# Kernel optimization log

Measured on AMD Instinct MI355X. Metric: run time of the kernel, lower is better.

## Reference

```python
import jax, jax.numpy as jnp
import numpy as np

B, T, D_MODEL, HEAD = 4, 4096, 1024, 64

def setup_inputs() -> dict:
    key = jax.random.key(0)
    ks = jax.random.split(key, 7)
    s = 0.02  # typical init scale
    return {
        "x":  jax.random.normal(ks[0], (B, T, D_MODEL), dtype=jnp.float32),
        "Wq": jax.random.normal(ks[1], (D_MODEL, HEAD), dtype=jnp.float32) * s,
        "bq": jnp.zeros((HEAD,), dtype=jnp.float32),
        "Wk": jax.random.normal(ks[2], (D_MODEL, HEAD), dtype=jnp.float32) * s,
        "bk": jnp.zeros((HEAD,), dtype=jnp.float32),
        "Wv": jax.random.normal(ks[3], (D_MODEL, HEAD), dtype=jnp.float32) * s,
        "bv": jnp.zeros((HEAD,), dtype=jnp.float32),
    }

def reference(x, Wq, bq, Wk, bk, Wv, bv):
    Bz, Tz, C = x.shape
    q = x @ Wq + bq                      # (B,T,H)
    k = x @ Wk + bk                      # (B,T,H)
    v = x @ Wv + bv                      # (B,T,H)
    # NOTE: original scales by sqrt(C) = sqrt(d_model), not sqrt(head_size)
    att = jnp.einsum("bth,bsh->bts", q, k) / jnp.sqrt(jnp.float32(C))
    causal = jnp.tril(jnp.ones((Tz, Tz), dtype=bool))
    att = jnp.where(causal, att, -jnp.inf)
    att = jax.nn.softmax(att, axis=-1)
    return jnp.einsum("bts,bsh->bth", att, v)  # (B,T,H)
```

## Files before the change

kernel.cpp:

```cpp
#include <hip/hip_runtime.h>
#include <hip/hip_bf16.h>
#include <hip/hip_fp16.h>

#define T_SEQ 4096
#define DMODEL 1024
#define HEAD 64
#define NBATCH 4
#define NSEG 576
#define S2LOG 0.04508422f

typedef __attribute__((ext_vector_type(8))) short bf16x8;
typedef __attribute__((ext_vector_type(4))) float f32x4;

__device__ __forceinline__ unsigned short f2bf(float f) {
    unsigned int b = __float_as_uint(f);
    unsigned int r = b + 0x7FFFu + ((b >> 16) & 1u);
    return (unsigned short)(r >> 16);
}
__device__ __forceinline__ unsigned int pk_bf16(float a, float b) {
    __hip_bfloat162 h = __float22bfloat162_rn(make_float2(a, b));
    unsigned int u; __builtin_memcpy(&u, &h, 4); return u;
}

__global__ __launch_bounds__(256) void prep_w(
    const float* __restrict__ Wq, const float* __restrict__ Wk,
    const float* __restrict__ Wv, unsigned short* __restrict__ Wtb)
{
    __shared__ unsigned short tl[64 * 72];
    const int bid = blockIdx.x;
    const int m   = bid >> 4;
    const int k0  = (bid & 15) * 64;
    const float* W = (m == 0) ? Wq : (m == 1) ? Wk : Wv;
    const int t  = threadIdx.x;
    const int kr = t >> 2, qtr = t & 3;
#pragma unroll
    for (int i = 0; i < 4; ++i) {
        float4 wv4 = *(const float4*)&W[(k0 + kr) * 64 + qtr * 16 + i * 4];
        tl[(qtr * 16 + i * 4 + 0) * 72 + kr] = f2bf(wv4.x);
        tl[(qtr * 16 + i * 4 + 1) * 72 + kr] = f2bf(wv4.y);
        tl[(qtr * 16 + i * 4 + 2) * 72 + kr] = f2bf(wv4.z);
        tl[(qtr * 16 + i * 4 + 3) * 72 + kr] = f2bf(wv4.w);
    }
    __syncthreads();
#pragma unroll
    for (int c = 0; c < 2; ++c) {
        const int lin = c * 256 + t;
        const int n = lin >> 3, k8 = lin & 7;
        *(uint4*)&Wtb[((long)(m * 64 + n)) * 1024 + k0 + k8 * 8] =
            *(const uint4*)&tl[n * 72 + k8 * 8];
    }
}

__global__ __launch_bounds__(256, 2) void qkv_mfma(
    const float* __restrict__ x, const unsigned short* __restrict__ Wtb,
    const float* __restrict__ bq, const float* __restrict__ bk,
    const float* __restrict__ bv,
    unsigned short* __restrict__ qo, unsigned short* __restrict__ ko,
    unsigned short* __restrict__ vt)
{
    __shared__ __align__(16) unsigned short x_s[2][32 * 136];
    const int t    = threadIdx.x;
    const int lane = t & 63;
    const int l15  = lane & 15, quad = lane >> 4;
    const int w    = __builtin_amdgcn_readfirstlane(t >> 6);
    const long row0 = (long)blockIdx.x * 32;

    float bias[3];
#pragma unroll
    for (int ntl = 0; ntl < 3; ++ntl) {
        const int c = w * 48 + ntl * 16 + l15;
        bias[ntl] = (c < 64) ? bq[c] : (c < 128) ? bk[c - 64] : bv[c - 128];
    }
    f32x4 acc[2][3];
#pragma unroll
    for (int mt = 0; mt < 2; ++mt)
#pragma unroll
        for (int ntl = 0; ntl < 3; ++ntl)
            acc[mt][ntl] = (f32x4){bias[ntl], bias[ntl], bias[ntl], bias[ntl]};

    const int srow = t >> 3, sseg = t & 7;
    const float* xp = x + (row0 + srow) * DMODEL + sseg * 16;

    float4 xv[4];
#pragma unroll
    for (int i = 0; i < 4; ++i) xv[i] = *(const float4*)(xp + i * 4);
    {
        unsigned int pk_[8];
#pragma unroll
        for (int i = 0; i < 4; ++i) {
            pk_[i * 2]     = pk_bf16(xv[i].x, xv[i].y);
            pk_[i * 2 + 1] = pk_bf16(xv[i].z, xv[i].w);
        }
        *(uint4*)&x_s[0][srow * 136 + sseg * 16]     = *(const uint4*)&pk_[0];
        *(uint4*)&x_s[0][srow * 136 + sseg * 16 + 8] = *(const uint4*)&pk_[4];
    }
    __syncthreads();

    for (int sg = 0; sg < 8; ++sg) {
        if (sg + 1 < 8)
#pragma unroll
            for (int i = 0; i < 4; ++i)
                xv[i] = *(const float4*)(xp + (sg + 1) * 128 + i * 4);
        bf16x8 wf[3][4];
#pragma unroll
        for (int ntl = 0; ntl < 3; ++ntl)
#pragma unroll
            for (int kq = 0; kq < 4; ++kq)
                wf[ntl][kq] = *(const bf16x8*)&Wtb[((long)(w * 48 + ntl * 16 + l15)) * 1024
                                                   + sg * 128 + kq * 32 + quad * 8];
#pragma unroll
        for (int mt = 0; mt < 2; ++mt)
#pragma unroll
            for (int kq = 0; kq < 4; ++kq) {
                bf16x8 a = *(const bf16x8*)&x_s[sg & 1][(mt * 16 + l15) * 136 + kq * 32 + quad * 8];
#pragma unroll
                for (int ntl = 0; ntl < 3; ++ntl)
                    acc[mt][ntl] = __builtin_amdgcn_mfma_f32_16x16x32_bf16(a, wf[ntl][kq], acc[mt][ntl], 0, 0, 0);
            }
        if (sg + 1 < 8) {
            unsigned int pk_[8];
#pragma unroll
            for (int i = 0; i < 4; ++i) {
                pk_[i * 2]     = pk_bf16(xv[i].x, xv[i].y);
                pk_[i * 2 + 1] = pk_bf16(xv[i].z, xv[i].w);
            }
            *(uint4*)&x_s[(sg + 1) & 1][srow * 136 + sseg * 16]     = *(const uint4*)&pk_[0];
            *(uint4*)&x_s[(sg + 1) & 1][srow * 136 + sseg * 16 + 8] = *(const uint4*)&pk_[4];
        }
        __syncthreads();
    }
#pragma unroll
    for (int mt = 0; mt < 2; ++mt)
#pragma unroll
        for (int ntl = 0; ntl < 3; ++ntl) {
            const int c = w * 48 + ntl * 16 + l15;
            const long tr0 = row0 + mt * 16 + quad * 4;
            if (c < 64) {
#pragma unroll
                for (int r = 0; r < 4; ++r)
                    qo[(tr0 + r) * HEAD + c] = f2bf(acc[mt][ntl][r] * S2LOG);
            } else if (c < 128) {
#pragma unroll
                for (int r = 0; r < 4; ++r)
                    ko[(tr0 + r) * HEAD + (c - 64)] = f2bf(acc[mt][ntl][r]);
            } else {
                const int b = (int)(tr0 >> 12), tloc = (int)(tr0 & 4095);
                uint2 pv;
                pv.x = pk_bf16(acc[mt][ntl][0], acc[mt][ntl][1]);
                pv.y = pk_bf16(acc[mt][ntl][2], acc[mt][ntl][3]);
                *(uint2*)&vt[((long)(b * HEAD + (c - 128))) * T_SEQ + tloc] = pv;
            }
        }
}

__global__ __launch_bounds__(256, 3) void flash_seg(
    const unsigned short* __restrict__ qg,
    const unsigned short* __restrict__ kg,
    const unsigned short* __restrict__ vtg,
    __half* __restrict__ opart, float* __restrict__ ml)
{
    __shared__ __align__(16) unsigned short p_s[4][32 * 72];
    const int t0   = threadIdx.x;
    const int lane = t0 & 63;
    const int l15  = lane & 15, quad = lane >> 4;
    const int wv   = __builtin_amdgcn_readfirstlane(t0 >> 6);

    const int sid = (NSEG - 1) - (int)blockIdx.x;
    int kk = 0, pref = 0;
#pragma unroll
    for (int i = 0; i < 7; ++i) {
        const int cnt = 16 * (kk + 1);
        if (sid >= pref + cnt) { pref += cnt; ++kk; }
    }
    const int S   = kk + 1;
    const int rem = sid - pref;
    const int t   = kk * 16 + rem / S;
    const int si  = rem % S;
    const int r0  = t * 32;
    const int nck = (t + 2) >> 1;
    const int c0  = (si * nck) / S, c1 = ((si + 1) * nck) / S;
    const int b   = wv;
    const long bbase = (long)b * T_SEQ;
    const int gidx = b * NSEG + sid;

    bf16x8 qf[2][2];
#pragma unroll
    for (int s = 0; s < 2; ++s)
#pragma unroll
        for (int h = 0; h < 2; ++h)
            qf[s][h] = *(const bf16x8*)&qg[(bbase + r0 + s * 16 + l15) * HEAD + h * 32 + quad * 8];

    f32x4 o[2][4];
#pragma unroll
    for (int s = 0; s < 2; ++s)
#pragma unroll
        for (int dt = 0; dt < 4; ++dt) o[s][dt] = (f32x4){0.f, 0.f, 0.f, 0.f};
    float mrun[2] = {-30000.f, -30000.f}, lrun[2] = {0.f, 0.f};

    unsigned short* ps = p_s[wv];

    for (int c = c0; c < c1; ++c) {
        const int key0 = c * 64;
        bf16x8 kf[4][2];
#pragma unroll
        for (int mt = 0; mt < 4; ++mt) {
            int krow = key0 + mt * 16 + l15; if (krow > T_SEQ - 1) krow = T_SEQ - 1;
            const unsigned short* kp = &kg[(bbase + krow) * HEAD + quad * 8];
            kf[mt][0] = *(const bf16x8*)kp;
            kf[mt][1] = *(const bf16x8*)(kp + 32);
        }
        f32x4 st[2][4];
#pragma unroll
        for (int s = 0; s < 2; ++s)
#pragma unroll
            for (int mt = 0; mt < 4; ++mt) {
                f32x4 z = (f32x4){0.f, 0.f, 0.f, 0.f};
                z = __builtin_amdgcn_mfma_f32_16x16x32_bf16(kf[mt][0], qf[s][0], z, 0, 0, 0);
                st[s][mt] = __builtin_amdgcn_mfma_f32_16x16x32_bf16(kf[mt][1], qf[s][1], z, 0, 0, 0);
            }
        bf16x8 vf[4][2];
#pragma unroll
        for (int dt = 0; dt < 4; ++dt)
#pragma unroll
            for (int g = 0; g < 2; ++g) {
                int kof = key0 + g * 32 + quad * 8; if (kof > T_SEQ - 8) kof = T_SEQ - 8;
                vf[dt][g] = *(const bf16x8*)&vtg[((long)(b * HEAD + dt * 16 + l15)) * T_SEQ + kof];
            }
        if (key0 + 63 > r0) {
#pragma unroll
            for (int s = 0; s < 2; ++s) {
                const int row = r0 + s * 16 + l15;
#pragma unroll
                for (int mt = 0; mt < 4; ++mt)
#pragma unroll
                    for (int r = 0; r < 4; ++r) {
                        const int key = key0 + mt * 16 + quad * 4 + r;
                        st[s][mt][r] = (key <= row) ? st[s][mt][r] : -30000.f;
                    }
            }
        }
#pragma unroll
        for (int s = 0; s < 2; ++s) {
            float mx = st[s][0][0];
#pragma unroll
            for (int mt = 0; mt < 4; ++mt)
#pragma unroll
                for (int r = 0; r < 4; ++r) mx = fmaxf(mx, st[s][mt][r]);
            mx = fmaxf(mx, __shfl_xor(mx, 16));
            mx = fmaxf(mx, __shfl_xor(mx, 32));
            const float mn = fmaxf(mrun[s], mx);
            const float al = exp2f(mrun[s] - mn);
            mrun[s] = mn;
            float psum = 0.f;
#pragma unroll
            for (int mt = 0; mt < 4; ++mt) {
                float e0 = exp2f(st[s][mt][0] - mn), e1 = exp2f(st[s][mt][1] - mn);
                float e2 = exp2f(st[s][mt][2] - mn), e3 = exp2f(st[s][mt][3] - mn);
                psum += (e0 + e1) + (e2 + e3);
                *(unsigned int*)&ps[(s * 16 + l15) * 72 + mt * 16 + quad * 4]     = pk_bf16(e0, e1);
                *(unsigned int*)&ps[(s * 16 + l15) * 72 + mt * 16 + quad * 4 + 2] = pk_bf16(e2, e3);
            }
            psum += __shfl_xor(psum, 16);
            psum += __shfl_xor(psum, 32);
            lrun[s] = lrun[s] * al + psum;
#pragma unroll
            for (int dt = 0; dt < 4; ++dt)
#pragma unroll
                for (int r = 0; r < 4; ++r) o[s][dt][r] *= al;
        }
        __builtin_amdgcn_wave_barrier();
        bf16x8 pf[2][2];
#pragma unroll
        for (int s = 0; s < 2; ++s)
#pragma unroll
            for (int g = 0; g < 2; ++g)
                pf[s][g] = *(const bf16x8*)&ps[(s * 16 + l15) * 72 + g * 32 + quad * 8];
        __builtin_amdgcn_wave_barrier();
#pragma unroll
        for (int s = 0; s < 2; ++s)
#pragma unroll
            for (int dt = 0; dt < 4; ++dt) {
                o[s][dt] = __builtin_amdgcn_mfma_f32_16x16x32_bf16(vf[dt][0], pf[s][0], o[s][dt], 0, 0, 0);
                o[s][dt] = __builtin_amdgcn_mfma_f32_16x16x32_bf16(vf[dt][1], pf[s][1], o[s][dt], 0, 0, 0);
            }
    }
    __half* op = opart + (long)gidx * 2048;
#pragma unroll
    for (int s = 0; s < 2; ++s) {
#pragma unroll
        for (int dt = 0; dt < 4; ++dt) {
            __half2 h0 = __floats2half2_rn(o[s][dt][0], o[s][dt][1]);
            __half2 h1 = __floats2half2_rn(o[s][dt][2], o[s][dt][3]);
            uint2 u; __builtin_memcpy(&u.x, &h0, 4); __builtin_memcpy(&u.y, &h1, 4);
            *(uint2*)&op[(s * 16 + l15) * HEAD + dt * 16 + quad * 4] = u;
        }
        if (quad == 0) {
            ml[(long)gidx * 64 + s * 16 + l15]      = mrun[s];
            ml[(long)gidx * 64 + 32 + s * 16 + l15] = lrun[s];
        }
    }
}

__global__ __launch_bounds__(256) void merge_seg(
    const __half* __restrict__ opart, const float* __restrict__ ml,
    float* __restrict__ out)
{
    const int bid = blockIdx.x;
    const int t = bid & 127, b = bid >> 7;
    const int kk = t >> 4, S = kk + 1;
    const int base_sid = 8 * kk * (kk + 1) + (t & 15) * S;
    const int tid = threadIdx.x;
    const int row = tid >> 3, col0 = (tid & 7) * 8;

    float m[8], l[8], M = -30000.f;
    for (int si = 0; si < S; ++si) {
        const long g = (long)(b * NSEG + base_sid + si);
        m[si] = ml[g * 64 + row];
        l[si] = ml[g * 64 + 32 + row];
        M = fmaxf(M, m[si]);
    }
    float acc[8];
#pragma unroll
    for (int j = 0; j < 8; ++j) acc[j] = 0.f;
    float L = 0.f;
    for (int si = 0; si < S; ++si) {
        const float wgt = exp2f(m[si] - M);
        L += wgt * l[si];
        const __half* op = opart + (long)(b * NSEG + base_sid + si) * 2048 + row * 64 + col0;
        uint4 u = *(const uint4*)op;
        __half2 h01, h23, h45, h67;
        __builtin_memcpy(&h01, &u.x, 4); __builtin_memcpy(&h23, &u.y, 4);
        __builtin_memcpy(&h45, &u.z, 4); __builtin_memcpy(&h67, &u.w, 4);
        float2 f01 = __half22float2(h01), f23 = __half22float2(h23);
        float2 f45 = __half22float2(h45), f67 = __half22float2(h67);
        acc[0] += wgt * f01.x; acc[1] += wgt * f01.y;
        acc[2] += wgt * f23.x; acc[3] += wgt * f23.y;
        acc[4] += wgt * f45.x; acc[5] += wgt * f45.y;
        acc[6] += wgt * f67.x; acc[7] += wgt * f67.y;
    }
    const float inv = 1.f / L;
    float4 o0 = {acc[0] * inv, acc[1] * inv, acc[2] * inv, acc[3] * inv};
    float4 o1 = {acc[4] * inv, acc[5] * inv, acc[6] * inv, acc[7] * inv};
    float* dst = out + ((long)(b * T_SEQ + t * 32 + row)) * HEAD + col0;
    *(float4*)dst = o0;
    *(float4*)(dst + 4) = o1;
}

extern "C" void kernel_launch(void* const* d_in, const int* in_sizes, int n_in,
                              void* d_out, int out_size, void* d_ws, size_t ws_size,
                              hipStream_t stream) {
    const float* x  = (const float*)d_in[0];
    const float* Wq = (const float*)d_in[1];
    const float* bq = (const float*)d_in[2];
    const float* Wk = (const float*)d_in[3];
    const float* bk = (const float*)d_in[4];
    const float* Wv = (const float*)d_in[5];
    const float* bv = (const float*)d_in[6];
    float* outp = (float*)d_out;

    char* wsb = (char*)d_ws;
    unsigned short* wtb = (unsigned short*)(wsb);
    unsigned short* qw  = (unsigned short*)(wsb + 393216);
    unsigned short* kw  = (unsigned short*)(wsb + 2490368);
    unsigned short* vtw = (unsigned short*)(wsb + 4587520);
    __half* opart       = (__half*)(wsb + 6684672);
    float*  mlp         = (float*)(wsb + 16121856);

    prep_w<<<dim3(48), dim3(256), 0, stream>>>(Wq, Wk, Wv, wtb);
    qkv_mfma<<<dim3(512), dim3(256), 0, stream>>>(
        x, wtb, bq, bk, bv, qw, kw, vtw);
    flash_seg<<<dim3(NSEG), dim3(256), 0, stream>>>(qw, kw, vtw, opart, mlp);
    merge_seg<<<dim3(512), dim3(256), 0, stream>>>(opart, mlp, outp);
}
```

Measured before the change: 177.3 us.

## Stage x and K/V tiles via direct global-to-LDS DMA and retile flash attention

```diff
diff --git a/kernel.cpp b/kernel.cpp
--- a/kernel.cpp
+++ b/kernel.cpp
@@ -6,7 +6,7 @@
 #define DMODEL 1024
 #define HEAD 64
 #define NBATCH 4
-#define NSEG 576
+#define NSEG 544
 #define S2LOG 0.04508422f
 
 typedef __attribute__((ext_vector_type(8))) short bf16x8;
@@ -20,6 +20,11 @@
 __device__ __forceinline__ unsigned int pk_bf16(float a, float b) {
     __hip_bfloat162 h = __float22bfloat162_rn(make_float2(a, b));
     unsigned int u; __builtin_memcpy(&u, &h, 4); return u;
+}
+__device__ __forceinline__ void dma16(const void* g, void* s) {
+    __builtin_amdgcn_global_load_lds(
+        (const __attribute__((address_space(1))) unsigned int*)g,
+        (__attribute__((address_space(3))) unsigned int*)s, 16, 0, 0);
 }
 
 __global__ __launch_bounds__(256) void prep_w(
@@ -51,14 +56,14 @@
     }
 }
 
-__global__ __launch_bounds__(256, 2) void qkv_mfma(
+__global__ __launch_bounds__(256, 3) void qkv_mfma(
     const float* __restrict__ x, const unsigned short* __restrict__ Wtb,
     const float* __restrict__ bq, const float* __restrict__ bk,
     const float* __restrict__ bv,
     unsigned short* __restrict__ qo, unsigned short* __restrict__ ko,
     unsigned short* __restrict__ vt)
 {
-    __shared__ __align__(16) unsigned short x_s[2][32 * 136];
+    __shared__ __align__(16) float xs[2][4096];
     const int t    = threadIdx.x;
     const int lane = t & 63;
     const int l15  = lane & 15, quad = lane >> 4;
@@ -78,29 +83,21 @@
         for (int ntl = 0; ntl < 3; ++ntl)
             acc[mt][ntl] = (f32x4){bias[ntl], bias[ntl], bias[ntl], bias[ntl]};
 
-    const int srow = t >> 3, sseg = t & 7;
-    const float* xp = x + (row0 + srow) * DMODEL + sseg * 16;
-
-    float4 xv[4];
-#pragma unroll
-    for (int i = 0; i < 4; ++i) xv[i] = *(const float4*)(xp + i * 4);
-    {
-        unsigned int pk_[8];
+    auto dma_stage = [&](int sg, int buf) {
 #pragma unroll
         for (int i = 0; i < 4; ++i) {
-            pk_[i * 2]     = pk_bf16(xv[i].x, xv[i].y);
-            pk_[i * 2 + 1] = pk_bf16(xv[i].z, xv[i].w);
-        }
-        *(uint4*)&x_s[0][srow * 136 + sseg * 16]     = *(const uint4*)&pk_[0];
-        *(uint4*)&x_s[0][srow * 136 + sseg * 16 + 8] = *(const uint4*)&pk_[4];
-    }
-    __syncthreads();
+            const int jj  = w * 4 + i;
+            const int row = jj * 2 + (lane >> 5);
+            const int lgb = (lane & 31) ^ (row & 7);
+            dma16(x + (row0 + row) * DMODEL + sg * 128 + lgb * 4,
+                  &xs[buf][jj * 256]);
+        }
+    };
+    dma_stage(0, 0);
 
     for (int sg = 0; sg < 8; ++sg) {
-        if (sg + 1 < 8)
-#pragma unroll
-            for (int i = 0; i < 4; ++i)
-                xv[i] = *(const float4*)(xp + (sg + 1) * 128 + i * 4);
+        __syncthreads();
+        if (sg + 1 < 8) dma_stage(sg + 1, (sg + 1) & 1);
         bf16x8 wf[3][4];
 #pragma unroll
         for (int ntl = 0; ntl < 3; ++ntl)
@@ -112,22 +109,19 @@
         for (int mt = 0; mt < 2; ++mt)
 #pragma unroll
             for (int kq = 0; kq < 4; ++kq) {
-                bf16x8 a = *(const bf16x8*)&x_s[sg & 1][(mt * 16 + l15) * 136 + kq * 32 + quad * 8];
+                const int row  = mt * 16 + l15;
+                const int b0   = (kq * 8 + quad * 2)     ^ (row & 7);
+                const int b1   = (kq * 8 + quad * 2 + 1) ^ (row & 7);
+                float4 a0 = *(const float4*)&xs[sg & 1][row * 128 + b0 * 4];
+                float4 a1 = *(const float4*)&xs[sg & 1][row * 128 + b1 * 4];
+                unsigned int u[4];
+                u[0] = pk_bf16(a0.x, a0.y); u[1] = pk_bf16(a0.z, a0.w);
+                u[2] = pk_bf16(a1.x, a1.y); u[3] = pk_bf16(a1.z, a1.w);
+                bf16x8 a; __builtin_memcpy(&a, u, 16);
 #pragma unroll
                 for (int ntl = 0; ntl < 3; ++ntl)
                     acc[mt][ntl] = __builtin_amdgcn_mfma_f32_16x16x32_bf16(a, wf[ntl][kq], acc[mt][ntl], 0, 0, 0);
             }
-        if (sg + 1 < 8) {
-            unsigned int pk_[8];
-#pragma unroll
-            for (int i = 0; i < 4; ++i) {
-                pk_[i * 2]     = pk_bf16(xv[i].x, xv[i].y);
-                pk_[i * 2 + 1] = pk_bf16(xv[i].z, xv[i].w);
-            }
-            *(uint4*)&x_s[(sg + 1) & 1][srow * 136 + sseg * 16]     = *(const uint4*)&pk_[0];
-            *(uint4*)&x_s[(sg + 1) & 1][srow * 136 + sseg * 16 + 8] = *(const uint4*)&pk_[4];
-        }
-        __syncthreads();
     }
 #pragma unroll
     for (int mt = 0; mt < 2; ++mt)
@@ -159,145 +153,148 @@
     const unsigned short* __restrict__ vtg,
     __half* __restrict__ opart, float* __restrict__ ml)
 {
-    __shared__ __align__(16) unsigned short p_s[4][32 * 72];
+    __shared__ __align__(16) unsigned short kv_s[2][8192];
+    __shared__ __align__(16) unsigned short p_s[4][16 * 72];
     const int t0   = threadIdx.x;
     const int lane = t0 & 63;
     const int l15  = lane & 15, quad = lane >> 4;
     const int wv   = __builtin_amdgcn_readfirstlane(t0 >> 6);
 
-    const int sid = (NSEG - 1) - (int)blockIdx.x;
+    const int bid = (int)blockIdx.x;
+    const int sid = (NSEG - 1) - (bid >> 2);
+    const int b   = bid & 3;
+
     int kk = 0, pref = 0;
 #pragma unroll
-    for (int i = 0; i < 7; ++i) {
-        const int cnt = 16 * (kk + 1);
+    for (int i = 0; i < 15; ++i) {
+        const int cnt = 4 * (kk + 1);
         if (sid >= pref + cnt) { pref += cnt; ++kk; }
     }
     const int S   = kk + 1;
     const int rem = sid - pref;
-    const int t   = kk * 16 + rem / S;
+    const int t   = kk * 4 + rem / S;
     const int si  = rem % S;
-    const int r0  = t * 32;
-    const int nck = (t + 2) >> 1;
+    const int r0  = t * 64;
+    const int rw  = r0 + wv * 16;
+    const int nck = t + 1;
     const int c0  = (si * nck) / S, c1 = ((si + 1) * nck) / S;
-    const int b   = wv;
     const long bbase = (long)b * T_SEQ;
     const int gidx = b * NSEG + sid;
 
-    bf16x8 qf[2][2];
-#pragma unroll
-    for (int s = 0; s < 2; ++s)
-#pragma unroll
-        for (int h = 0; h < 2; ++h)
-            qf[s][h] = *(const bf16x8*)&qg[(bbase + r0 + s * 16 + l15) * HEAD + h * 32 + quad * 8];
-
-    f32x4 o[2][4];
-#pragma unroll
-    for (int s = 0; s < 2; ++s)
-#pragma unroll
-        for (int dt = 0; dt < 4; ++dt) o[s][dt] = (f32x4){0.f, 0.f, 0.f, 0.f};
-    float mrun[2] = {-30000.f, -30000.f}, lrun[2] = {0.f, 0.f};
-
+    bf16x8 qf[2];
+#pragma unroll
+    for (int h = 0; h < 2; ++h)
+        qf[h] = *(const bf16x8*)&qg[(bbase + rw + l15) * HEAD + h * 32 + quad * 8];
+
+    f32x4 o[4];
+#pragma unroll
+    for (int dt = 0; dt < 4; ++dt) o[dt] = (f32x4){0.f, 0.f, 0.f, 0.f};
+    float mrun = -30000.f, lrun = 0.f;
     unsigned short* ps = p_s[wv];
+
+    auto dma_chunk = [&](int key0, int buf) {
+#pragma unroll
+        for (int i = 0; i < 2; ++i) {
+            const int jj  = wv * 2 + i;
+            const int kl  = jj * 8 + (lane >> 3);
+            const int dlg = (lane & 7) ^ ((lane >> 3) & 7);
+            dma16(kg + (bbase + key0 + kl) * HEAD + dlg * 8,
+                  &kv_s[buf][jj * 512]);
+        }
+#pragma unroll
+        for (int i = 0; i < 2; ++i) {
+            const int jj  = wv * 2 + i;
+            const int dim = jj * 8 + (lane >> 3);
+            const int klg = (lane & 7) ^ ((lane >> 3) & 7);
+            dma16(vtg + ((long)(b * HEAD + dim)) * T_SEQ + key0 + klg * 8,
+                  &kv_s[buf][4096 + jj * 512]);
+        }
+    };
+    dma_chunk(c0 * 64, 0);
 
     for (int c = c0; c < c1; ++c) {
         const int key0 = c * 64;
-        bf16x8 kf[4][2];
+        const int cur  = (c - c0) & 1;
+        __syncthreads();
+        if (c + 1 < c1) dma_chunk((c + 1) * 64, cur ^ 1);
+
+        f32x4 st[4];
 #pragma unroll
         for (int mt = 0; mt < 4; ++mt) {
-            int krow = key0 + mt * 16 + l15; if (krow > T_SEQ - 1) krow = T_SEQ - 1;
-            const unsigned short* kp = &kg[(bbase + krow) * HEAD + quad * 8];
-            kf[mt][0] = *(const bf16x8*)kp;
-            kf[mt][1] = *(const bf16x8*)(kp + 32);
-        }
-        f32x4 st[2][4];
-#pragma unroll
-        for (int s = 0; s < 2; ++s)
-#pragma unroll
-            for (int mt = 0; mt < 4; ++mt) {
-                f32x4 z = (f32x4){0.f, 0.f, 0.f, 0.f};
-                z = __builtin_amdgcn_mfma_f32_16x16x32_bf16(kf[mt][0], qf[s][0], z, 0, 0, 0);
-                st[s][mt] = __builtin_amdgcn_mfma_f32_16x16x32_bf16(kf[mt][1], qf[s][1], z, 0, 0, 0);
-            }
+            const int key_l = mt * 16 + l15;
+            bf16x8 k0 = *(const bf16x8*)&kv_s[cur][key_l * 64 + ((quad    ) ^ (l15 & 7)) * 8];
+            bf16x8 k1 = *(const bf16x8*)&kv_s[cur][key_l * 64 + ((quad + 4) ^ (l15 & 7)) * 8];
+            f32x4 z = (f32x4){0.f, 0.f, 0.f, 0.f};
+            z = __builtin_amdgcn_mfma_f32_16x16x32_bf16(k0, qf[0], z, 0, 0, 0);
+            st[mt] = __builtin_amdgcn_mfma_f32_16x16x32_bf16(k1, qf[1], st[mt] = z, 0, 0, 0);
+        }
         bf16x8 vf[4][2];
 #pragma unroll
+        for (int dt = 0; dt < 4; ++dt) {
+            const int dim = dt * 16 + l15;
+            vf[dt][0] = *(const bf16x8*)&kv_s[cur][4096 + dim * 64 + ((quad    ) ^ (l15 & 7)) * 8];
+            vf[dt][1] = *(const bf16x8*)&kv_s[cur][4096 + dim * 64 + ((quad + 4) ^ (l15 & 7)) * 8];
+        }
+        if (key0 + 63 > rw) {
+            const int row = rw + l15;
+#pragma unroll
+            for (int mt = 0; mt < 4; ++mt)
+#pragma unroll
+                for (int r = 0; r < 4; ++r) {
+                    const int key = key0 + mt * 16 + quad * 4 + r;
+                    st[mt][r] = (key <= row) ? st[mt][r] : -30000.f;
+                }
+        }
+        float mx = st[0][0];
+#pragma unroll
+        for (int mt = 0; mt < 4; ++mt)
+#pragma unroll
+            for (int r = 0; r < 4; ++r) mx = fmaxf(mx, st[mt][r]);
+        mx = fmaxf(mx, __shfl_xor(mx, 16));
+        mx = fmaxf(mx, __shfl_xor(mx, 32));
+        const float mn = fmaxf(mrun, mx);
+        const float al = exp2f(mrun - mn);
+        mrun = mn;
+        float psum = 0.f;
+#pragma unroll
+        for (int mt = 0; mt < 4; ++mt) {
+            float e0 = exp2f(st[mt][0] - mn), e1 = exp2f(st[mt][1] - mn);
+            float e2 = exp2f(st[mt][2] - mn), e3 = exp2f(st[mt][3] - mn);
+            psum += (e0 + e1) + (e2 + e3);
+            *(unsigned int*)&ps[l15 * 72 + mt * 16 + quad * 4]     = pk_bf16(e0, e1);
+            *(unsigned int*)&ps[l15 * 72 + mt * 16 + quad * 4 + 2] = pk_bf16(e2, e3);
+        }
+        psum += __shfl_xor(psum, 16);
+        psum += __shfl_xor(psum, 32);
+        lrun = lrun * al + psum;
+#pragma unroll
         for (int dt = 0; dt < 4; ++dt)
 #pragma unroll
-            for (int g = 0; g < 2; ++g) {
-                int kof = key0 + g * 32 + quad * 8; if (kof > T_SEQ - 8) kof = T_SEQ - 8;
-                vf[dt][g] = *(const bf16x8*)&vtg[((long)(b * HEAD + dt * 16 + l15)) * T_SEQ + kof];
-            }
-        if (key0 + 63 > r0) {
-#pragma unroll
-            for (int s = 0; s < 2; ++s) {
-                const int row = r0 + s * 16 + l15;
-#pragma unroll
-                for (int mt = 0; mt < 4; ++mt)
-#pragma unroll
-                    for (int r = 0; r < 4; ++r) {
-                        const int key = key0 + mt * 16 + quad * 4 + r;
-                        st[s][mt][r] = (key <= row) ? st[s][mt][r] : -30000.f;
-                    }
-            }
-        }
-#pragma unroll
-        for (int s = 0; s < 2; ++s) {
-            float mx = st[s][0][0];
-#pragma unroll
-            for (int mt = 0; mt < 4; ++mt)
-#pragma unroll
-                for (int r = 0; r < 4; ++r) mx = fmaxf(mx, st[s][mt][r]);
-            mx = fmaxf(mx, __shfl_xor(mx, 16));
-            mx = fmaxf(mx, __shfl_xor(mx, 32));
-            const float mn = fmaxf(mrun[s], mx);
-            const float al = exp2f(mrun[s] - mn);
-            mrun[s] = mn;
-            float psum = 0.f;
-#pragma unroll
-            for (int mt = 0; mt < 4; ++mt) {
-                float e0 = exp2f(st[s][mt][0] - mn), e1 = exp2f(st[s][mt][1] - mn);
-                float e2 = exp2f(st[s][mt][2] - mn), e3 = exp2f(st[s][mt][3] - mn);
-                psum += (e0 + e1) + (e2 + e3);
-                *(unsigned int*)&ps[(s * 16 + l15) * 72 + mt * 16 + quad * 4]     = pk_bf16(e0, e1);
-                *(unsigned int*)&ps[(s * 16 + l15) * 72 + mt * 16 + quad * 4 + 2] = pk_bf16(e2, e3);
-            }
-            psum += __shfl_xor(psum, 16);
-            psum += __shfl_xor(psum, 32);
-            lrun[s] = lrun[s] * al + psum;
-#pragma unroll
-            for (int dt = 0; dt < 4; ++dt)
-#pragma unroll
-                for (int r = 0; r < 4; ++r) o[s][dt][r] *= al;
-        }
+            for (int r = 0; r < 4; ++r) o[dt][r] *= al;
         __builtin_amdgcn_wave_barrier();
-        bf16x8 pf[2][2];
-#pragma unroll
-        for (int s = 0; s < 2; ++s)
-#pragma unroll
-            for (int g = 0; g < 2; ++g)
-                pf[s][g] = *(const bf16x8*)&ps[(s * 16 + l15) * 72 + g * 32 + quad * 8];
+        bf16x8 pf[2];
+#pragma unroll
+        for (int g = 0; g < 2; ++g)
+            pf[g] = *(const bf16x8*)&ps[l15 * 72 + g * 32 + quad * 8];
         __builtin_amdgcn_wave_barrier();
 #pragma unroll
-        for (int s = 0; s < 2; ++s)
-#pragma unroll
-            for (int dt = 0; dt < 4; ++dt) {
-                o[s][dt] = __builtin_amdgcn_mfma_f32_16x16x32_bf16(vf[dt][0], pf[s][0], o[s][dt], 0, 0, 0);
-                o[s][dt] = __builtin_amdgcn_mfma_f32_16x16x32_bf16(vf[dt][1], pf[s][1], o[s][dt], 0, 0, 0);
-            }
-    }
-    __half* op = opart + (long)gidx * 2048;
-#pragma unroll
-    for (int s = 0; s < 2; ++s) {
-#pragma unroll
         for (int dt = 0; dt < 4; ++dt) {
-            __half2 h0 = __floats2half2_rn(o[s][dt][0], o[s][dt][1]);
-            __half2 h1 = __floats2half2_rn(o[s][dt][2], o[s][dt][3]);
-            uint2 u; __builtin_memcpy(&u.x, &h0, 4); __builtin_memcpy(&u.y, &h1, 4);
-            *(uint2*)&op[(s * 16 + l15) * HEAD + dt * 16 + quad * 4] = u;
-        }
-        if (quad == 0) {
-            ml[(long)gidx * 64 + s * 16 + l15]      = mrun[s];
-            ml[(long)gidx * 64 + 32 + s * 16 + l15] = lrun[s];
-        }
+            o[dt] = __builtin_amdgcn_mfma_f32_16x16x32_bf16(vf[dt][0], pf[0], o[dt], 0, 0, 0);
+            o[dt] = __builtin_amdgcn_mfma_f32_16x16x32_bf16(vf[dt][1], pf[1], o[dt], 0, 0, 0);
+        }
+    }
+
+    __half* op = opart + (long)gidx * 4096;
+#pragma unroll
+    for (int dt = 0; dt < 4; ++dt) {
+        __half2 h0 = __floats2half2_rn(o[dt][0], o[dt][1]);
+        __half2 h1 = __floats2half2_rn(o[dt][2], o[dt][3]);
+        uint2 u; __builtin_memcpy(&u.x, &h0, 4); __builtin_memcpy(&u.y, &h1, 4);
+        *(uint2*)&op[(wv * 16 + l15) * HEAD + dt * 16 + quad * 4] = u;
+    }
+    if (quad == 0) {
+        ml[(long)gidx * 128 + wv * 16 + l15]      = mrun;
+        ml[(long)gidx * 128 + 64 + wv * 16 + l15] = lrun;
     }
 }
 
@@ -306,44 +303,47 @@
     float* __restrict__ out)
 {
     const int bid = blockIdx.x;
-    const int t = bid & 127, b = bid >> 7;
-    const int kk = t >> 4, S = kk + 1;
-    const int base_sid = 8 * kk * (kk + 1) + (t & 15) * S;
+    const int t = bid & 63, b = bid >> 6;
+    const int kk = t >> 2, S = kk + 1;
+    const int base_sid = 2 * kk * (kk + 1) + (t & 3) * S;
     const int tid = threadIdx.x;
-    const int row = tid >> 3, col0 = (tid & 7) * 8;
-
-    float m[8], l[8], M = -30000.f;
+    const int row = tid >> 2, col0 = (tid & 3) * 16;
+
+    float M = -30000.f;
+    for (int si = 0; si < S; ++si)
+        M = fmaxf(M, ml[(long)(b * NSEG + base_sid + si) * 128 + row]);
+
+    float acc[16];
+#pragma unroll
+    for (int j = 0; j < 16; ++j) acc[j] = 0.f;
+    float L = 0.f;
     for (int si = 0; si < S; ++si) {
         const long g = (long)(b * NSEG + base_sid + si);
-        m[si] = ml[g * 64 + row];
-        l[si] = ml[g * 64 + 32 + row];
-        M = fmaxf(M, m[si]);
-    }
-    float acc[8];
-#pragma unroll
-    for (int j = 0; j < 8; ++j) acc[j] = 0.f;
-    float L = 0.f;
-    for (int si = 0; si < S; ++si) {
-        const float wgt = exp2f(m[si] - M);
-        L += wgt * l[si];
-        const __half* op = opart + (long)(b * NSEG + base_sid + si) * 2048 + row * 64 + col0;
-        uint4 u = *(const uint4*)op;
-        __half2 h01, h23, h45, h67;
-        __builtin_memcpy(&h01, &u.x, 4); __builtin_memcpy(&h23, &u.y, 4);
-        __builtin_memcpy(&h45, &u.z, 4); __builtin_memcpy(&h67, &u.w, 4);
-        float2 f01 = __half22float2(h01), f23 = __half22float2(h23);
-        float2 f45 = __half22float2(h45), f67 = __half22float2(h67);
-        acc[0] += wgt * f01.x; acc[1] += wgt * f01.y;
-        acc[2] += wgt * f23.x; acc[3] += wgt * f23.y;
-        acc[4] += wgt * f45.x; acc[5] += wgt * f45.y;
-        acc[6] += wgt * f67.x; acc[7] += wgt * f67.y;
+        const float wgt = exp2f(ml[g * 128 + row] - M);
+        L += wgt * ml[g * 128 + 64 + row];
+        const __half* op = opart + g * 4096 + row * 64 + col0;
+#pragma unroll
+        for (int h = 0; h < 2; ++h) {
+            uint4 u = *(const uint4*)(op + h * 8);
+            __half2 h01, h23, h45, h67;
+            __builtin_memcpy(&h01, &u.x, 4); __builtin_memcpy(&h23, &u.y, 4);
+            __builtin_memcpy(&h45, &u.z, 4); __builtin_memcpy(&h67, &u.w, 4);
+            float2 f01 = __half22float2(h01), f23 = __half22float2(h23);
+            float2 f45 = __half22float2(h45), f67 = __half22float2(h67);
+            acc[h * 8 + 0] += wgt * f01.x; acc[h * 8 + 1] += wgt * f01.y;
+            acc[h * 8 + 2] += wgt * f23.x; acc[h * 8 + 3] += wgt * f23.y;
+            acc[h * 8 + 4] += wgt * f45.x; acc[h * 8 + 5] += wgt * f45.y;
+            acc[h * 8 + 6] += wgt * f67.x; acc[h * 8 + 7] += wgt * f67.y;
+        }
     }
     const float inv = 1.f / L;
-    float4 o0 = {acc[0] * inv, acc[1] * inv, acc[2] * inv, acc[3] * inv};
-    float4 o1 = {acc[4] * inv, acc[5] * inv, acc[6] * inv, acc[7] * inv};
-    float* dst = out + ((long)(b * T_SEQ + t * 32 + row)) * HEAD + col0;
-    *(float4*)dst = o0;
-    *(float4*)(dst + 4) = o1;
+    float* dst = out + ((long)(b * T_SEQ + t * 64 + row)) * HEAD + col0;
+#pragma unroll
+    for (int h = 0; h < 4; ++h) {
+        float4 ov = {acc[h * 4] * inv, acc[h * 4 + 1] * inv,
+                     acc[h * 4 + 2] * inv, acc[h * 4 + 3] * inv};
+        *(float4*)(dst + h * 4) = ov;
+    }
 }
 
 extern "C" void kernel_launch(void* const* d_in, const int* in_sizes, int n_in,
@@ -364,11 +364,11 @@
     unsigned short* kw  = (unsigned short*)(wsb + 2490368);
     unsigned short* vtw = (unsigned short*)(wsb + 4587520);
     __half* opart       = (__half*)(wsb + 6684672);
-    float*  mlp         = (float*)(wsb + 16121856);
+    float*  mlp         = (float*)(wsb + 24510464);
 
     prep_w<<<dim3(48), dim3(256), 0, stream>>>(Wq, Wk, Wv, wtb);
     qkv_mfma<<<dim3(512), dim3(256), 0, stream>>>(
         x, wtb, bq, bk, bv, qw, kw, vtw);
-    flash_seg<<<dim3(NSEG), dim3(256), 0, stream>>>(qw, kw, vtw, opart, mlp);
-    merge_seg<<<dim3(512), dim3(256), 0, stream>>>(opart, mlp, outp);
-}
+    flash_seg<<<dim3(NSEG * NBATCH), dim3(256), 0, stream>>>(qw, kw, vtw, opart, mlp);
+    merge_seg<<<dim3(256), dim3(256), 0, stream>>>(opart, mlp, outp);
+}
```

Result: faster. 163.1 us (-8.0%).
